# Performance work log

Measured on AMD Instinct MI355X. Metric: run time of the kernel, lower is better.

The kernel has to match this reference:

```python
import jax, jax.numpy as jnp
import numpy as np

H = 16
D_MODEL = 1024
D_K = D_MODEL // H  # 64, must equal embeddim


def setup_inputs() -> dict:
    key = jax.random.key(0)
    ks = jax.random.split(key, 20)
    B, S, D = 4, 1024, D_MODEL
    s = 0.02
    inp = {
        'query': jax.random.normal(ks[0], (B, S, D), jnp.float32),
        'key':   jax.random.normal(ks[1], (B, S, D), jnp.float32),
        'value': jax.random.normal(ks[2], (B, S, D), jnp.float32),
        'mask':  jnp.ones((B, S, S), jnp.int32),
        # four d_model x d_model projections (q, k, v, out)
        'wq': jax.random.normal(ks[3], (D, D), jnp.float32) * s, 'bq': jnp.zeros((D,), jnp.float32),
        'wk': jax.random.normal(ks[4], (D, D), jnp.float32) * s, 'bk': jnp.zeros((D,), jnp.float32),
        'wv': jax.random.normal(ks[5], (D, D), jnp.float32) * s, 'bv': jnp.zeros((D,), jnp.float32),
        'wo': jax.random.normal(ks[6], (D, D), jnp.float32) * s, 'bo': jnp.zeros((D,), jnp.float32),
        # per-head (embeddim=64) linears
        'spatial_w': jax.random.normal(ks[7], (D_K, D_K), jnp.float32) * s, 'spatial_b': jnp.zeros((D_K,), jnp.float32),
        'qproj_w':   jax.random.normal(ks[8], (D_K, D_K), jnp.float32) * s, 'qproj_b':   jnp.zeros((D_K,), jnp.float32),
        'kproj_w':   jax.random.normal(ks[9], (D_K, D_K), jnp.float32) * s, 'kproj_b':   jnp.zeros((D_K,), jnp.float32),
        'vlin_w':    jax.random.normal(ks[10], (D_K, D_K), jnp.float32) * s, 'vlin_b':    jnp.zeros((D_K,), jnp.float32),
        # channel_linear: Linear(1, 64)
        'chan_w': jax.random.normal(ks[11], (1, D_K), jnp.float32) * s, 'chan_b': jnp.zeros((D_K,), jnp.float32),
    }
    return inp


def reference(query, key, value, mask,
              wq, bq, wk, bk, wv, bv, wo, bo,
              spatial_w, spatial_b, qproj_w, qproj_b,
              kproj_w, kproj_b, vlin_w, vlin_b, chan_w, chan_b):
    B, S, D = query.shape
    # project and split heads -> [B, H, S, D_K]
    def heads(x, w, b):
        return (x @ w + b).reshape(B, S, H, D_K).transpose(0, 2, 1, 3)
    q = heads(query, wq, bq)
    k = heads(key, wk, bk)
    v = heads(value, wv, bv)

    q = jax.nn.elu(q @ spatial_w + spatial_b)
    q_refine = q @ qproj_w + qproj_b
    # channel gate: mean over channels -> Linear(1,64) -> matmul with raw key
    alpha = q_refine.mean(-1, keepdims=True) @ chan_w + chan_b        # [B,H,S,64]
    gate = jax.nn.sigmoid(jnp.einsum('bhqe,bhke->bhqk', alpha, k))    # [B,H,S,S]

    k2 = jax.nn.elu(k @ kproj_w + kproj_b)
    scores = jnp.einsum('bhqe,bhke->bhqk', q, k2) / jnp.sqrt(jnp.asarray(D_K, q.dtype))
    scores = scores * gate
    scores = jnp.where(mask[:, None] == 0, jnp.asarray(-1e9, scores.dtype), scores)
    p_attn = jax.nn.softmax(scores, axis=-1)

    v2 = jax.nn.elu(v @ vlin_w + vlin_b)
    x = jnp.einsum('bhqk,bhke->bhqe', p_attn, v2)                     # [B,H,S,64]
    x = x.transpose(0, 2, 1, 3).reshape(B, S, H * D_K)
    return x @ wo + bo
```

## Files before the change

kernel.cpp:

```cpp
#include <hip/hip_runtime.h>
#include <math.h>

#define D_MODEL 1024
#define NH 16
#define DK 64
#define S_LEN 1024
#define BATCH 4
#define MROWS (BATCH * S_LEN)

typedef short bf16x8 __attribute__((ext_vector_type(8)));
typedef float f32x4 __attribute__((ext_vector_type(4)));
typedef unsigned short u16;

__device__ __forceinline__ float elu1(float x) {
    return x > 0.f ? x : (expf(x) - 1.f);
}

__device__ __forceinline__ u16 f2bf(float f) {
    union { float f; unsigned u; } v; v.f = f;
    unsigned u = v.u;
    return (u16)((u + 0x7fffu + ((u >> 16) & 1u)) >> 16);
}

__device__ __forceinline__ unsigned pack2(float a, float b) {
    union { float f; unsigned u; } ua, ub; ua.f = a; ub.f = b;
    return ((ua.u + 0x8000u) >> 16) | ((ub.u + 0x8000u) & 0xffff0000u);
}

__device__ __forceinline__ void async16(const void* g, void* l) {
    __builtin_amdgcn_global_load_lds(
        (const __attribute__((address_space(1))) unsigned int*)g,
        (__attribute__((address_space(3))) unsigned int*)l,
        16, 0, 0);
}

__global__ __launch_bounds__(256) void cast_wt(
    const float* __restrict__ wq, const float* __restrict__ wk,
    const float* __restrict__ wv, const float* __restrict__ wo,
    u16* __restrict__ WT)
{
    __shared__ float T[64][65];
    const int z = blockIdx.z;
    const float* W = (z == 0) ? wq : ((z == 1) ? wk : ((z == 2) ? wv : wo));
    u16* O = WT + (size_t)z * D_MODEL * D_MODEL;
    const int tid = threadIdx.x;
    const int k0 = blockIdx.y * 64, n0 = blockIdx.x * 64;
    const int r = tid >> 4, c4 = (tid & 15) * 4;
    #pragma unroll
    for (int p = 0; p < 4; p++) {
        float4 v = *(const float4*)&W[(size_t)(k0 + r + p * 16) * D_MODEL + n0 + c4];
        T[r + p * 16][c4 + 0] = v.x; T[r + p * 16][c4 + 1] = v.y;
        T[r + p * 16][c4 + 2] = v.z; T[r + p * 16][c4 + 3] = v.w;
    }
    __syncthreads();
    #pragma unroll
    for (int p = 0; p < 4; p++) {
        const int i = r + p * 16;
        ushort4 o4;
        o4.x = f2bf(T[c4 + 0][i]); o4.y = f2bf(T[c4 + 1][i]);
        o4.z = f2bf(T[c4 + 2][i]); o4.w = f2bf(T[c4 + 3][i]);
        *(ushort4*)&O[(size_t)(n0 + i) * D_MODEL + k0 + c4] = o4;
    }
}

__global__ __launch_bounds__(256) void proj_fused(
    const float* __restrict__ Xq, const float* __restrict__ Xk, const float* __restrict__ Xv,
    const u16* __restrict__ WTq, const u16* __restrict__ WTk, const u16* __restrict__ WTv,
    const float* __restrict__ bq, const float* __restrict__ bk, const float* __restrict__ bv,
    const float* __restrict__ spatial_w, const float* __restrict__ spatial_b,
    const float* __restrict__ qproj_w, const float* __restrict__ qproj_b,
    const float* __restrict__ kproj_w, const float* __restrict__ kproj_b,
    const float* __restrict__ vlin_w, const float* __restrict__ vlin_b,
    const float* __restrict__ chan_w, const float* __restrict__ chan_b,
    u16* __restrict__ Qh, u16* __restrict__ K2, u16* __restrict__ V2t,
    float* __restrict__ mB, float* __restrict__ uB, float* __restrict__ vB)
{
    __shared__ __align__(16) u16 smem[23040];
    __shared__ float auxA[64];
    __shared__ float auxS;

    u16* As = smem;
    u16* Bs = smem + 8192;
    u16* W2t = smem + 18432;

    const int z = blockIdx.z;
    const float* X = (z == 0) ? Xq : ((z == 1) ? Xk : Xv);
    const u16* WT = (z == 0) ? WTq : ((z == 1) ? WTk : WTv);
    const float* B1 = (z == 0) ? bq : ((z == 1) ? bk : bv);
    const float* W2 = (z == 0) ? spatial_w : ((z == 1) ? kproj_w : vlin_w);
    const float* B2 = (z == 0) ? spatial_b : ((z == 1) ? kproj_b : vlin_b);

    const int tid = threadIdx.x;
    const int wave = tid >> 6, lane = tid & 63;
    const int col = lane & 15, quad = lane >> 4;
    const int wr = wave >> 1, wc = wave & 1;
    const int r0 = blockIdx.x * 128, n0 = blockIdx.y * 128;
    const int hh = blockIdx.y * 2 + wc;

    #pragma unroll
    for (int p = 0; p < 4; p++) {
        int idx = p * 256 + tid;
        int f = idx >> 4, e4 = (idx & 15) * 4;
        float4 w4 = *(const float4*)&W2[f * 64 + e4];
        W2t[(e4 + 0) * 72 + f] = f2bf(w4.x);
        W2t[(e4 + 1) * 72 + f] = f2bf(w4.y);
        W2t[(e4 + 2) * 72 + f] = f2bf(w4.z);
        W2t[(e4 + 3) * 72 + f] = f2bf(w4.w);
    }
    if (z == 0) {
        {
            int row = tid >> 2, part = tid & 3;
            float s = 0.f;
            for (int e = part * 16; e < part * 16 + 16; e++) s += qproj_w[row * 64 + e];
            s += __shfl_xor(s, 1);
            s += __shfl_xor(s, 2);
            if (part == 0) auxA[row] = s * (1.f / 64.f);
        }
        if (tid < 64) {
            float s = qproj_b[tid];
            #pragma unroll
            for (int m = 1; m < 64; m <<= 1) s += __shfl_xor(s, m);
            if (tid == 0) auxS = s * (1.f / 64.f);
        }
    }

    const int arow = tid >> 1, ap = tid & 1;
    const float* aptr = X + (size_t)(r0 + arow) * D_MODEL + ap * 32;
    u16* adst = As + ap * 4096 + arow * 32;

    const int brow = lane >> 2, bseg = lane & 3;
    const u16* bp = WT + (size_t)(n0 + wave * 32 + brow) * D_MODEL + bseg * 8;
    u16* bd_l0 = Bs + (wave * 32) * 32;
    u16* bd_l1 = Bs + (wave * 32 + 16) * 32;
    u16* bd_h0 = Bs + 4096 + (wave * 32) * 32;
    u16* bd_h1 = Bs + 4096 + (wave * 32 + 16) * 32;

    f32x4 acc[4][4];
    #pragma unroll
    for (int i = 0; i < 4; i++)
        #pragma unroll
        for (int j = 0; j < 4; j++)
            acc[i][j] = (f32x4){0.f, 0.f, 0.f, 0.f};

    float4 fr[8];
    #pragma unroll
    for (int i = 0; i < 8; i++) fr[i] = *(const float4*)(aptr + i * 4);

    for (int k0 = 0; k0 < D_MODEL; k0 += 64) {
        if (k0) __syncthreads();
        async16(bp + k0, bd_l0);
        async16(bp + 16 * D_MODEL + k0, bd_l1);
        async16(bp + k0 + 32, bd_h0);
        async16(bp + 16 * D_MODEL + k0 + 32, bd_h1);
        {
            #pragma unroll
            for (int j = 0; j < 4; j++) {
                uint4 q;
                q.x = pack2(fr[2 * j].x, fr[2 * j].y);
                q.y = pack2(fr[2 * j].z, fr[2 * j].w);
                q.z = pack2(fr[2 * j + 1].x, fr[2 * j + 1].y);
                q.w = pack2(fr[2 * j + 1].z, fr[2 * j + 1].w);
                *(uint4*)(adst + j * 8) = q;
            }
        }
        if (k0 + 64 < D_MODEL) {
            const float* apn = aptr + k0 + 64;
            #pragma unroll
            for (int i = 0; i < 8; i++) fr[i] = *(const float4*)(apn + i * 4);
        }
        __syncthreads();
        const u16* Abase = As + (wr * 64 + col) * 32 + quad * 8;
        const u16* Bbase = Bs + (wc * 64 + col) * 32 + quad * 8;
        #pragma unroll
        for (int p = 0; p < 2; p++) {
            bf16x8 af[4], bfr[4];
            #pragma unroll
            for (int mi = 0; mi < 4; mi++) af[mi] = *(const bf16x8*)(Abase + p * 4096 + mi * 512);
            #pragma unroll
            for (int ni = 0; ni < 4; ni++) bfr[ni] = *(const bf16x8*)(Bbase + p * 4096 + ni * 512);
            #pragma unroll
            for (int mi = 0; mi < 4; mi++)
                #pragma unroll
                for (int ni = 0; ni < 4; ni++)
                    acc[mi][ni] = __builtin_amdgcn_mfma_f32_16x16x32_bf16(af[mi], bfr[ni], acc[mi][ni], 0, 0, 0);
        }
    }

    float b1v[4];
    #pragma unroll
    for (int ni = 0; ni < 4; ni++) b1v[ni] = B1[hh * 64 + ni * 16 + col];

    const int rbase = r0 + wr * 64;
    const int b = rbase >> 10;
    const int s0 = rbase & 1023;
    const size_t svecbase = ((size_t)b * NH + hh) * S_LEN;

    if (z == 1) {
        float cw[4], cb[4];
        #pragma unroll
        for (int ni = 0; ni < 4; ni++) { cw[ni] = chan_w[ni * 16 + col]; cb[ni] = chan_b[ni * 16 + col]; }
        #pragma unroll
        for (int mi = 0; mi < 4; mi++)
            #pragma unroll
            for (int r = 0; r < 4; r++) {
                float su = 0.f, sv = 0.f;
                #pragma unroll
                for (int ni = 0; ni < 4; ni++) {
                    float p = acc[mi][ni][r] + b1v[ni];
                    su += p * cw[ni];
                    sv += p * cb[ni];
                }
                su += __shfl_xor(su, 1); su += __shfl_xor(su, 2);
                su += __shfl_xor(su, 4); su += __shfl_xor(su, 8);
                sv += __shfl_xor(sv, 1); sv += __shfl_xor(sv, 2);
                sv += __shfl_xor(sv, 4); sv += __shfl_xor(sv, 8);
                if (col == 0) {
                    const size_t idx = svecbase + s0 + mi * 16 + quad * 4 + r;
                    uB[idx] = su;
                    vB[idx] = sv;
                }
            }
    }

    __syncthreads();

    u16* Pw = smem + wave * 4608;
    #pragma unroll
    for (int mi = 0; mi < 4; mi++)
        #pragma unroll
        for (int ni = 0; ni < 4; ni++)
            #pragma unroll
            for (int r = 0; r < 4; r++)
                Pw[(mi * 16 + quad * 4 + r) * 72 + ni * 16 + col] =
                    f2bf(acc[mi][ni][r] + b1v[ni]);

    __builtin_amdgcn_s_waitcnt(0xc07f);

    bf16x8 af2[4][2], bf2r[4][2];
    #pragma unroll
    for (int mi = 0; mi < 4; mi++) {
        af2[mi][0] = *(const bf16x8*)&Pw[(mi * 16 + col) * 72 + quad * 8];
        af2[mi][1] = *(const bf16x8*)&Pw[(mi * 16 + col) * 72 + 32 + quad * 8];
    }
    #pragma unroll
    for (int ni = 0; ni < 4; ni++) {
        bf2r[ni][0] = *(const bf16x8*)&W2t[(ni * 16 + col) * 72 + quad * 8];
        bf2r[ni][1] = *(const bf16x8*)&W2t[(ni * 16 + col) * 72 + 32 + quad * 8];
    }
    f32x4 out2[4][4];
    #pragma unroll
    for (int mi = 0; mi < 4; mi++)
        #pragma unroll
        for (int ni = 0; ni < 4; ni++) {
            f32x4 c = (f32x4){0.f, 0.f, 0.f, 0.f};
            c = __builtin_amdgcn_mfma_f32_16x16x32_bf16(af2[mi][0], bf2r[ni][0], c, 0, 0, 0);
            c = __builtin_amdgcn_mfma_f32_16x16x32_bf16(af2[mi][1], bf2r[ni][1], c, 0, 0, 0);
            out2[mi][ni] = c;
        }

    float b2v[4];
    #pragma unroll
    for (int ni = 0; ni < 4; ni++) b2v[ni] = B2[ni * 16 + col];
    float qs[4][4][4];
    #pragma unroll
    for (int mi = 0; mi < 4; mi++)
        #pragma unroll
        for (int ni = 0; ni < 4; ni++)
            #pragma unroll
            for (int r = 0; r < 4; r++)
                qs[mi][ni][r] = elu1(out2[mi][ni][r] + b2v[ni]);

    if (z == 0) {
        float aw[4];
        #pragma unroll
        for (int ni = 0; ni < 4; ni++) aw[ni] = auxA[ni * 16 + col];
        #pragma unroll
        for (int mi = 0; mi < 4; mi++)
            #pragma unroll
            for (int r = 0; r < 4; r++) {
                float pm = 0.f;
                #pragma unroll
                for (int ni = 0; ni < 4; ni++) pm += qs[mi][ni][r] * aw[ni];
                pm += __shfl_xor(pm, 1); pm += __shfl_xor(pm, 2);
                pm += __shfl_xor(pm, 4); pm += __shfl_xor(pm, 8);
                if (col == 0)
                    mB[svecbase + s0 + mi * 16 + quad * 4 + r] = pm + auxS;
            }
        #pragma unroll
        for (int mi = 0; mi < 4; mi++)
            #pragma unroll
            for (int ni = 0; ni < 4; ni++)
                #pragma unroll
                for (int r = 0; r < 4; r++)
                    Qh[(size_t)(rbase + mi * 16 + quad * 4 + r) * D_MODEL
                       + hh * 64 + ni * 16 + col] = f2bf(qs[mi][ni][r] * 0.125f);
    } else if (z == 1) {
        #pragma unroll
        for (int mi = 0; mi < 4; mi++)
            #pragma unroll
            for (int ni = 0; ni < 4; ni++)
                #pragma unroll
                for (int r = 0; r < 4; r++)
                    K2[(size_t)(rbase + mi * 16 + quad * 4 + r) * D_MODEL
                       + hh * 64 + ni * 16 + col] = f2bf(qs[mi][ni][r]);
    } else {
        __builtin_amdgcn_s_waitcnt(0xc07f);
        #pragma unroll
        for (int mi = 0; mi < 4; mi++)
            #pragma unroll
            for (int ni = 0; ni < 4; ni++)
                #pragma unroll
                for (int r = 0; r < 4; r++)
                    Pw[(ni * 16 + col) * 72 + mi * 16 + quad * 4 + r] = f2bf(qs[mi][ni][r]);
        __builtin_amdgcn_s_waitcnt(0xc07f);
        const int d = lane;
        u16* dst = V2t + (((size_t)b * NH + hh) * DK + d) * S_LEN + s0;
        const u16* srcp = Pw + d * 72;
        #pragma unroll
        for (int seg = 0; seg < 8; seg++)
            *(uint4*)(dst + seg * 8) = *(const uint4*)(srcp + seg * 8);
    }
}

__global__ __launch_bounds__(256) void attn_mfma(
    const u16* __restrict__ Qh, const u16* __restrict__ K2h, const u16* __restrict__ V2t,
    const float* __restrict__ Mq, const float* __restrict__ Uk, const float* __restrict__ Vk,
    const int* __restrict__ mask, u16* __restrict__ X)
{
    __shared__ u16 K2s[2][64][72];
    __shared__ u16 V2s[2][64][72];
    __shared__ u16 Ps[4][16][72];

    const int tid = threadIdx.x;
    const int wave = tid >> 6, lane = tid & 63;
    const int col = lane & 15, quad = lane >> 4;
    const int b = blockIdx.z, h = blockIdx.y;
    const int q0 = blockIdx.x * 64;
    const size_t hb = ((size_t)(b * NH + h)) * S_LEN * DK;
    const size_t sb = ((size_t)(b * NH + h)) * S_LEN;

    bf16x8 qf0, qf1;
    {
        const u16* qp = Qh + (size_t)(b * S_LEN + q0 + wave * 16 + col) * D_MODEL + h * 64 + quad * 8;
        qf0 = *(const bf16x8*)qp;
        qf1 = *(const bf16x8*)(qp + 32);
    }
    float mqv[4];
    #pragma unroll
    for (int r = 0; r < 4; r++)
        mqv[r] = Mq[sb + q0 + wave * 16 + quad * 4 + r];

    const int srow = tid >> 2, sseg = tid & 3;
    const u16* ksrc = K2h + (size_t)(b * S_LEN + srow) * D_MODEL + h * 64 + sseg * 16;
    const u16* vsrc = V2t + hb + (size_t)srow * S_LEN + sseg * 16;
    const int* mrow = mask + (size_t)b * S_LEN * S_LEN
                    + (size_t)(q0 + wave * 16 + quad * 4) * S_LEN + col;

    uint4 ka = *(const uint4*)(ksrc);
    uint4 kb = *(const uint4*)(ksrc + 8);
    uint4 va = *(const uint4*)(vsrc);
    uint4 vb = *(const uint4*)(vsrc + 8);
    float ku[4], kv[4];
    int mk[4][4];
    #pragma unroll
    for (int nb = 0; nb < 4; nb++) {
        ku[nb] = Uk[sb + nb * 16 + col];
        kv[nb] = Vk[sb + nb * 16 + col];
        #pragma unroll
        for (int r = 0; r < 4; r++) mk[nb][r] = mrow[(size_t)r * S_LEN + nb * 16];
    }

    float psum[4] = {0.f, 0.f, 0.f, 0.f};
    f32x4 o[4];
    #pragma unroll
    for (int nb = 0; nb < 4; nb++) o[nb] = (f32x4){0.f, 0.f, 0.f, 0.f};

    for (int t = 0; t < 16; t++) {
        const int bsel = t & 1;
        *(uint4*)&K2s[bsel][srow][sseg * 16]     = ka;
        *(uint4*)&K2s[bsel][srow][sseg * 16 + 8] = kb;
        *(uint4*)&V2s[bsel][srow][sseg * 16]     = va;
        *(uint4*)&V2s[bsel][srow][sseg * 16 + 8] = vb;
        __syncthreads();

        float kun[4], kvn[4];
        int mkn[4][4];
        if (t < 15) {
            const int k1 = (t + 1) * 64;
            const u16* ks = ksrc + (size_t)k1 * D_MODEL;
            const u16* vs = vsrc + k1;
            ka = *(const uint4*)(ks);
            kb = *(const uint4*)(ks + 8);
            va = *(const uint4*)(vs);
            vb = *(const uint4*)(vs + 8);
            #pragma unroll
            for (int nb = 0; nb < 4; nb++) {
                kun[nb] = Uk[sb + k1 + nb * 16 + col];
                kvn[nb] = Vk[sb + k1 + nb * 16 + col];
                #pragma unroll
                for (int r = 0; r < 4; r++)
                    mkn[nb][r] = mrow[k1 + (size_t)r * S_LEN + nb * 16];
            }
        }

        f32x4 sc[4];
        #pragma unroll
        for (int nb = 0; nb < 4; nb++) {
            bf16x8 b0 = *(const bf16x8*)&K2s[bsel][nb * 16 + col][quad * 8];
            bf16x8 b1 = *(const bf16x8*)&K2s[bsel][nb * 16 + col][32 + quad * 8];
            f32x4 c = (f32x4){0.f, 0.f, 0.f, 0.f};
            c = __builtin_amdgcn_mfma_f32_16x16x32_bf16(qf0, b0, c, 0, 0, 0);
            c = __builtin_amdgcn_mfma_f32_16x16x32_bf16(qf1, b1, c, 0, 0, 0);
            sc[nb] = c;
        }

        #pragma unroll
        for (int nb = 0; nb < 4; nb++) {
            #pragma unroll
            for (int r = 0; r < 4; r++) {
                float g = 1.f / (1.f + __expf(-(mqv[r] * ku[nb] + kv[nb])));
                float sv = sc[nb][r] * g;
                sv = mk[nb][r] ? sv : -30.f;
                float p = __expf(sv);
                psum[r] += p;
                Ps[wave][quad * 4 + r][nb * 16 + col] = f2bf(p);
            }
        }
        __builtin_amdgcn_s_waitcnt(0xc07f);
        bf16x8 a0 = *(const bf16x8*)&Ps[wave][col][quad * 8];
        bf16x8 a1 = *(const bf16x8*)&Ps[wave][col][32 + quad * 8];

        #pragma unroll
        for (int nb = 0; nb < 4; nb++) {
            bf16x8 b0 = *(const bf16x8*)&V2s[bsel][nb * 16 + col][quad * 8];
            bf16x8 b1 = *(const bf16x8*)&V2s[bsel][nb * 16 + col][32 + quad * 8];
            o[nb] = __builtin_amdgcn_mfma_f32_16x16x32_bf16(a0, b0, o[nb], 0, 0, 0);
            o[nb] = __builtin_amdgcn_mfma_f32_16x16x32_bf16(a1, b1, o[nb], 0, 0, 0);
        }

        if (t < 15) {
            #pragma unroll
            for (int nb = 0; nb < 4; nb++) {
                ku[nb] = kun[nb]; kv[nb] = kvn[nb];
                #pragma unroll
                for (int r = 0; r < 4; r++) mk[nb][r] = mkn[nb][r];
            }
        }
    }

    #pragma unroll
    for (int r = 0; r < 4; r++) {
        float t = psum[r];
        t += __shfl_xor(t, 1);
        t += __shfl_xor(t, 2);
        t += __shfl_xor(t, 4);
        t += __shfl_xor(t, 8);
        float inv = 1.f / t;
        u16* xp = X + (size_t)(b * S_LEN + q0 + wave * 16 + quad * 4 + r) * D_MODEL + h * 64 + col;
        #pragma unroll
        for (int nb = 0; nb < 4; nb++)
            xp[nb * 16] = f2bf(o[nb][r] * inv);
    }
}

__global__ __launch_bounds__(256) void out_gemm(
    const u16* __restrict__ A, const u16* __restrict__ WT,
    const float* __restrict__ bias, float* __restrict__ C)
{
    __shared__ u16 As[128 * 32];
    __shared__ u16 Bs[128 * 32];

    const int tid = threadIdx.x;
    const int wave = tid >> 6, lane = tid & 63;
    const int col = lane & 15, quad = lane >> 4;
    const int wr = wave >> 1, wc = wave & 1;
    const int r0 = blockIdx.x * 128, n0 = blockIdx.y * 128;

    const int ch0 = 2 * wave, ch1 = 2 * wave + 1;
    const u16* aptr0 = A + (size_t)(r0 + ch0 * 16 + (lane >> 2)) * D_MODEL + (lane & 3) * 8;
    const u16* aptr1 = A + (size_t)(r0 + ch1 * 16 + (lane >> 2)) * D_MODEL + (lane & 3) * 8;
    const u16* bptr0 = WT + (size_t)(n0 + ch0 * 16 + (lane >> 2)) * D_MODEL + (lane & 3) * 8;
    const u16* bptr1 = WT + (size_t)(n0 + ch1 * 16 + (lane >> 2)) * D_MODEL + (lane & 3) * 8;
    u16* adst0 = As + ch0 * 512;
    u16* adst1 = As + ch1 * 512;
    u16* bdst0 = Bs + ch0 * 512;
    u16* bdst1 = Bs + ch1 * 512;

    f32x4 acc[4][4];
    #pragma unroll
    for (int i = 0; i < 4; i++)
        #pragma unroll
        for (int j = 0; j < 4; j++)
            acc[i][j] = (f32x4){0.f, 0.f, 0.f, 0.f};

    for (int k0 = 0; k0 < D_MODEL; k0 += 32) {
        if (k0) __syncthreads();
        async16(aptr0 + k0, adst0);
        async16(aptr1 + k0, adst1);
        async16(bptr0 + k0, bdst0);
        async16(bptr1 + k0, bdst1);
        __syncthreads();
        const u16* Ab = As + (wr * 64 + col) * 32 + quad * 8;
        const u16* Bb = Bs + (wc * 64 + col) * 32 + quad * 8;
        bf16x8 af[4], bfr[4];
        #pragma unroll
        for (int mi = 0; mi < 4; mi++) af[mi] = *(const bf16x8*)(Ab + mi * 512);
        #pragma unroll
        for (int ni = 0; ni < 4; ni++) bfr[ni] = *(const bf16x8*)(Bb + ni * 512);
        #pragma unroll
        for (int mi = 0; mi < 4; mi++)
            #pragma unroll
            for (int ni = 0; ni < 4; ni++)
                acc[mi][ni] = __builtin_amdgcn_mfma_f32_16x16x32_bf16(af[mi], bfr[ni], acc[mi][ni], 0, 0, 0);
    }

    #pragma unroll
    for (int mi = 0; mi < 4; mi++)
        #pragma unroll
        for (int ni = 0; ni < 4; ni++) {
            const int gr = r0 + wr * 64 + mi * 16 + quad * 4;
            const int gc = n0 + wc * 64 + ni * 16 + col;
            const float bb = bias[gc];
            #pragma unroll
            for (int r = 0; r < 4; r++)
                C[(size_t)(gr + r) * D_MODEL + gc] = acc[mi][ni][r] + bb;
        }
}

extern "C" void kernel_launch(void* const* d_in, const int* in_sizes, int n_in,
                              void* d_out, int out_size, void* d_ws, size_t ws_size,
                              hipStream_t stream) {
    (void)in_sizes; (void)n_in; (void)out_size; (void)ws_size;
    const float* query = (const float*)d_in[0];
    const float* key_  = (const float*)d_in[1];
    const float* value = (const float*)d_in[2];
    const int*   mask  = (const int*)d_in[3];
    const float* wq = (const float*)d_in[4];  const float* bq = (const float*)d_in[5];
    const float* wk = (const float*)d_in[6];  const float* bk = (const float*)d_in[7];
    const float* wv = (const float*)d_in[8];  const float* bv = (const float*)d_in[9];
    const float* wo = (const float*)d_in[10]; const float* bo = (const float*)d_in[11];
    const float* spatial_w = (const float*)d_in[12]; const float* spatial_b = (const float*)d_in[13];
    const float* qproj_w   = (const float*)d_in[14]; const float* qproj_b   = (const float*)d_in[15];
    const float* kproj_w   = (const float*)d_in[16]; const float* kproj_b   = (const float*)d_in[17];
    const float* vlin_w    = (const float*)d_in[18]; const float* vlin_b    = (const float*)d_in[19];
    const float* chan_w    = (const float*)d_in[20]; const float* chan_b    = (const float*)d_in[21];
    float* out = (float*)d_out;

    char* ws = (char*)d_ws;
    u16* Qh  = (u16*)ws;
    u16* K2  = (u16*)(ws + ((size_t)8  << 20));
    u16* Xb  = (u16*)(ws + ((size_t)16 << 20));
    u16* WT  = (u16*)(ws + ((size_t)24 << 20));
    u16* V2t = (u16*)(ws + ((size_t)32 << 20));
    float* mB = (float*)(ws + ((size_t)40 << 20));
    float* uB = mB + (size_t)BATCH * NH * S_LEN;
    float* vB = uB + (size_t)BATCH * NH * S_LEN;
    const size_t WSZ = (size_t)D_MODEL * D_MODEL;

    cast_wt<<<dim3(16, 16, 4), 256, 0, stream>>>(wq, wk, wv, wo, WT);
    proj_fused<<<dim3(32, 8, 3), 256, 0, stream>>>(query, key_, value,
        WT, WT + WSZ, WT + 2 * WSZ, bq, bk, bv,
        spatial_w, spatial_b, qproj_w, qproj_b, kproj_w, kproj_b,
        vlin_w, vlin_b, chan_w, chan_b,
        Qh, K2, V2t, mB, uB, vB);
    attn_mfma<<<dim3(S_LEN / 64, NH, BATCH), 256, 0, stream>>>(Qh, K2, V2t, mB, uB, vB, mask, Xb);
    out_gemm<<<dim3(32, 8), 256, 0, stream>>>(Xb, WT + 3 * WSZ, bo, out);
}
```

Baseline: 317.3 us.

## Replace async LDS loads with register-prefetched tiles and widen out_gemm K-step

Drops the global_load_lds async copies in the projection GEMM and the output GEMM. Each thread now loads the next K-tile of weights and activations into registers after the barrier, so the global loads overlap the MFMA work on the current tile, then writes them to LDS at the top of the next iteration. out_gemm also moves from 32-wide to 64-wide K-steps, which halves its barrier count and doubles its LDS tiles. The cost is more register pressure and an explicit LDS store pass in place of direct-to-LDS loads.

```diff
diff --git a/kernel.cpp b/kernel.cpp
--- a/kernel.cpp
+++ b/kernel.cpp
@@ -25,13 +25,6 @@
 __device__ __forceinline__ unsigned pack2(float a, float b) {
     union { float f; unsigned u; } ua, ub; ua.f = a; ub.f = b;
     return ((ua.u + 0x8000u) >> 16) | ((ub.u + 0x8000u) & 0xffff0000u);
-}
-
-__device__ __forceinline__ void async16(const void* g, void* l) {
-    __builtin_amdgcn_global_load_lds(
-        (const __attribute__((address_space(1))) unsigned int*)g,
-        (__attribute__((address_space(3))) unsigned int*)l,
-        16, 0, 0);
 }
 
 __global__ __launch_bounds__(256) void cast_wt(
@@ -128,12 +121,8 @@
     const float* aptr = X + (size_t)(r0 + arow) * D_MODEL + ap * 32;
     u16* adst = As + ap * 4096 + arow * 32;
 
-    const int brow = lane >> 2, bseg = lane & 3;
-    const u16* bp = WT + (size_t)(n0 + wave * 32 + brow) * D_MODEL + bseg * 8;
-    u16* bd_l0 = Bs + (wave * 32) * 32;
-    u16* bd_l1 = Bs + (wave * 32 + 16) * 32;
-    u16* bd_h0 = Bs + 4096 + (wave * 32) * 32;
-    u16* bd_h1 = Bs + 4096 + (wave * 32 + 16) * 32;
+    const u16* bsrc = WT + (size_t)(n0 + arow) * D_MODEL + ap * 32;
+    u16* bdst = Bs + ap * 4096 + arow * 32;
 
     f32x4 acc[4][4];
     #pragma unroll
@@ -143,32 +132,36 @@
             acc[i][j] = (f32x4){0.f, 0.f, 0.f, 0.f};
 
     float4 fr[8];
+    uint4 bu[4];
     #pragma unroll
     for (int i = 0; i < 8; i++) fr[i] = *(const float4*)(aptr + i * 4);
+    #pragma unroll
+    for (int i = 0; i < 4; i++) bu[i] = *(const uint4*)(bsrc + i * 8);
 
     for (int k0 = 0; k0 < D_MODEL; k0 += 64) {
         if (k0) __syncthreads();
-        async16(bp + k0, bd_l0);
-        async16(bp + 16 * D_MODEL + k0, bd_l1);
-        async16(bp + k0 + 32, bd_h0);
-        async16(bp + 16 * D_MODEL + k0 + 32, bd_h1);
-        {
-            #pragma unroll
-            for (int j = 0; j < 4; j++) {
-                uint4 q;
-                q.x = pack2(fr[2 * j].x, fr[2 * j].y);
-                q.y = pack2(fr[2 * j].z, fr[2 * j].w);
-                q.z = pack2(fr[2 * j + 1].x, fr[2 * j + 1].y);
-                q.w = pack2(fr[2 * j + 1].z, fr[2 * j + 1].w);
-                *(uint4*)(adst + j * 8) = q;
-            }
-        }
+        #pragma unroll
+        for (int j = 0; j < 4; j++) {
+            uint4 q;
+            q.x = pack2(fr[2 * j].x, fr[2 * j].y);
+            q.y = pack2(fr[2 * j].z, fr[2 * j].w);
+            q.z = pack2(fr[2 * j + 1].x, fr[2 * j + 1].y);
+            q.w = pack2(fr[2 * j + 1].z, fr[2 * j + 1].w);
+            *(uint4*)(adst + j * 8) = q;
+        }
+        #pragma unroll
+        for (int i = 0; i < 4; i++) *(uint4*)(bdst + i * 8) = bu[i];
+        __syncthreads();
+
         if (k0 + 64 < D_MODEL) {
             const float* apn = aptr + k0 + 64;
             #pragma unroll
             for (int i = 0; i < 8; i++) fr[i] = *(const float4*)(apn + i * 4);
-        }
-        __syncthreads();
+            const u16* bpn = bsrc + k0 + 64;
+            #pragma unroll
+            for (int i = 0; i < 4; i++) bu[i] = *(const uint4*)(bpn + i * 8);
+        }
+
         const u16* Abase = As + (wr * 64 + col) * 32 + quad * 8;
         const u16* Bbase = Bs + (wc * 64 + col) * 32 + quad * 8;
         #pragma unroll
@@ -467,8 +460,8 @@
     const u16* __restrict__ A, const u16* __restrict__ WT,
     const float* __restrict__ bias, float* __restrict__ C)
 {
-    __shared__ u16 As[128 * 32];
-    __shared__ u16 Bs[128 * 32];
+    __shared__ u16 As[8192];
+    __shared__ u16 Bs[8192];
 
     const int tid = threadIdx.x;
     const int wave = tid >> 6, lane = tid & 63;
@@ -476,15 +469,11 @@
     const int wr = wave >> 1, wc = wave & 1;
     const int r0 = blockIdx.x * 128, n0 = blockIdx.y * 128;
 
-    const int ch0 = 2 * wave, ch1 = 2 * wave + 1;
-    const u16* aptr0 = A + (size_t)(r0 + ch0 * 16 + (lane >> 2)) * D_MODEL + (lane & 3) * 8;
-    const u16* aptr1 = A + (size_t)(r0 + ch1 * 16 + (lane >> 2)) * D_MODEL + (lane & 3) * 8;
-    const u16* bptr0 = WT + (size_t)(n0 + ch0 * 16 + (lane >> 2)) * D_MODEL + (lane & 3) * 8;
-    const u16* bptr1 = WT + (size_t)(n0 + ch1 * 16 + (lane >> 2)) * D_MODEL + (lane & 3) * 8;
-    u16* adst0 = As + ch0 * 512;
-    u16* adst1 = As + ch1 * 512;
-    u16* bdst0 = Bs + ch0 * 512;
-    u16* bdst1 = Bs + ch1 * 512;
+    const int arow = tid >> 1, ap = tid & 1;
+    const u16* asrc = A + (size_t)(r0 + arow) * D_MODEL + ap * 32;
+    const u16* bsrc = WT + (size_t)(n0 + arow) * D_MODEL + ap * 32;
+    u16* adst = As + ap * 4096 + arow * 32;
+    u16* bdst = Bs + ap * 4096 + arow * 32;
 
     f32x4 acc[4][4];
     #pragma unroll
@@ -493,25 +482,44 @@
         for (int j = 0; j < 4; j++)
             acc[i][j] = (f32x4){0.f, 0.f, 0.f, 0.f};
 
-    for (int k0 = 0; k0 < D_MODEL; k0 += 32) {
+    uint4 au[4], bu[4];
+    #pragma unroll
+    for (int i = 0; i < 4; i++) au[i] = *(const uint4*)(asrc + i * 8);
+    #pragma unroll
+    for (int i = 0; i < 4; i++) bu[i] = *(const uint4*)(bsrc + i * 8);
+
+    for (int k0 = 0; k0 < D_MODEL; k0 += 64) {
         if (k0) __syncthreads();
-        async16(aptr0 + k0, adst0);
-        async16(aptr1 + k0, adst1);
-        async16(bptr0 + k0, bdst0);
-        async16(bptr1 + k0, bdst1);
+        #pragma unroll
+        for (int i = 0; i < 4; i++) *(uint4*)(adst + i * 8) = au[i];
+        #pragma unroll
+        for (int i = 0; i < 4; i++) *(uint4*)(bdst + i * 8) = bu[i];
         __syncthreads();
-        const u16* Ab = As + (wr * 64 + col) * 32 + quad * 8;
-        const u16* Bb = Bs + (wc * 64 + col) * 32 + quad * 8;
-        bf16x8 af[4], bfr[4];
-        #pragma unroll
-        for (int mi = 0; mi < 4; mi++) af[mi] = *(const bf16x8*)(Ab + mi * 512);
-        #pragma unroll
-        for (int ni = 0; ni < 4; ni++) bfr[ni] = *(const bf16x8*)(Bb + ni * 512);
-        #pragma unroll
-        for (int mi = 0; mi < 4; mi++)
-            #pragma unroll
-            for (int ni = 0; ni < 4; ni++)
-                acc[mi][ni] = __builtin_amdgcn_mfma_f32_16x16x32_bf16(af[mi], bfr[ni], acc[mi][ni], 0, 0, 0);
+
+        if (k0 + 64 < D_MODEL) {
+            const u16* apn = asrc + k0 + 64;
+            const u16* bpn = bsrc + k0 + 64;
+            #pragma unroll
+            for (int i = 0; i < 4; i++) au[i] = *(const uint4*)(apn + i * 8);
+            #pragma unroll
+            for (int i = 0; i < 4; i++) bu[i] = *(const uint4*)(bpn + i * 8);
+        }
+
+        const u16* Abase = As + (wr * 64 + col) * 32 + quad * 8;
+        const u16* Bbase = Bs + (wc * 64 + col) * 32 + quad * 8;
+        #pragma unroll
+        for (int p = 0; p < 2; p++) {
+            bf16x8 af[4], bfr[4];
+            #pragma unroll
+            for (int mi = 0; mi < 4; mi++) af[mi] = *(const bf16x8*)(Abase + p * 4096 + mi * 512);
+            #pragma unroll
+            for (int ni = 0; ni < 4; ni++) bfr[ni] = *(const bf16x8*)(Bbase + p * 4096 + ni * 512);
+            #pragma unroll
+            for (int mi = 0; mi < 4; mi++)
+                #pragma unroll
+                for (int ni = 0; ni < 4; ni++)
+                    acc[mi][ni] = __builtin_amdgcn_mfma_f32_16x16x32_bf16(af[mi], bfr[ni], acc[mi][ni], 0, 0, 0);
+        }
     }
 
     #pragma unroll
```

After: 375.4 us. +18.3%, slower.

## Shrink projection and output GEMM tiles to raise block count and occupancy

Applied to the files above, without the earlier changes.

The fused projection kernel now computes a 128x64 tile per block (one head) instead of 128x128, with K-step 32 and smaller LDS. The per-head 64x64 linear and the V transpose are reworked to process 16-row chunks per wave and stage through shared memory in two passes. The output GEMM goes from 128x128 tiles to 64x64 tiles, launching four times as many blocks. This is meant to improve occupancy and wave count on the many-CU GPU, at the cost of less data reuse per block and more barriers per K step.

```diff
diff --git a/kernel.cpp b/kernel.cpp
--- a/kernel.cpp
+++ b/kernel.cpp
@@ -75,13 +75,13 @@
     u16* __restrict__ Qh, u16* __restrict__ K2, u16* __restrict__ V2t,
     float* __restrict__ mB, float* __restrict__ uB, float* __restrict__ vB)
 {
-    __shared__ __align__(16) u16 smem[23040];
+    __shared__ __align__(16) u16 smem[10752];
     __shared__ float auxA[64];
     __shared__ float auxS;
 
     u16* As = smem;
-    u16* Bs = smem + 8192;
-    u16* W2t = smem + 18432;
+    u16* Bs = smem + 4096;
+    u16* W2t = smem + 6144;
 
     const int z = blockIdx.z;
     const float* X = (z == 0) ? Xq : ((z == 1) ? Xk : Xv);
@@ -93,9 +93,9 @@
     const int tid = threadIdx.x;
     const int wave = tid >> 6, lane = tid & 63;
     const int col = lane & 15, quad = lane >> 4;
-    const int wr = wave >> 1, wc = wave & 1;
-    const int r0 = blockIdx.x * 128, n0 = blockIdx.y * 128;
-    const int hh = blockIdx.y * 2 + wc;
+    const int r0 = blockIdx.x * 128;
+    const int hh = blockIdx.y;
+    const int n0 = hh * 64;
 
     #pragma unroll
     for (int p = 0; p < 4; p++) {
@@ -124,75 +124,63 @@
         }
     }
 
-    const int arow = tid >> 1, ap = tid & 1;
-    const float* aptr = X + (size_t)(r0 + arow) * D_MODEL + ap * 32;
-    u16* adst = As + ap * 4096 + arow * 32;
-
-    const int brow = lane >> 2, bseg = lane & 3;
-    const u16* bp = WT + (size_t)(n0 + wave * 32 + brow) * D_MODEL + bseg * 8;
-    u16* bd_l0 = Bs + (wave * 32) * 32;
-    u16* bd_l1 = Bs + (wave * 32 + 16) * 32;
-    u16* bd_h0 = Bs + 4096 + (wave * 32) * 32;
-    u16* bd_h1 = Bs + 4096 + (wave * 32 + 16) * 32;
-
-    f32x4 acc[4][4];
-    #pragma unroll
-    for (int i = 0; i < 4; i++)
+    const int arow = tid >> 1, ahalf = tid & 1;
+    const float* aptr = X + (size_t)(r0 + arow) * D_MODEL + ahalf * 16;
+    u16* adst = As + arow * 32 + ahalf * 16;
+
+    const u16* bp = WT + (size_t)(n0 + wave * 16 + (lane >> 2)) * D_MODEL + (lane & 3) * 8;
+    u16* bdst = Bs + wave * 16 * 32;
+
+    f32x4 acc[2][4];
+    #pragma unroll
+    for (int i = 0; i < 2; i++)
         #pragma unroll
         for (int j = 0; j < 4; j++)
             acc[i][j] = (f32x4){0.f, 0.f, 0.f, 0.f};
 
-    float4 fr[8];
-    #pragma unroll
-    for (int i = 0; i < 8; i++) fr[i] = *(const float4*)(aptr + i * 4);
-
-    for (int k0 = 0; k0 < D_MODEL; k0 += 64) {
+    float4 fr[4];
+    #pragma unroll
+    for (int i = 0; i < 4; i++) fr[i] = *(const float4*)(aptr + i * 4);
+
+    for (int k0 = 0; k0 < D_MODEL; k0 += 32) {
         if (k0) __syncthreads();
-        async16(bp + k0, bd_l0);
-        async16(bp + 16 * D_MODEL + k0, bd_l1);
-        async16(bp + k0 + 32, bd_h0);
-        async16(bp + 16 * D_MODEL + k0 + 32, bd_h1);
+        async16(bp + k0, bdst);
         {
-            #pragma unroll
-            for (int j = 0; j < 4; j++) {
-                uint4 q;
-                q.x = pack2(fr[2 * j].x, fr[2 * j].y);
-                q.y = pack2(fr[2 * j].z, fr[2 * j].w);
-                q.z = pack2(fr[2 * j + 1].x, fr[2 * j + 1].y);
-                q.w = pack2(fr[2 * j + 1].z, fr[2 * j + 1].w);
-                *(uint4*)(adst + j * 8) = q;
-            }
-        }
-        if (k0 + 64 < D_MODEL) {
-            const float* apn = aptr + k0 + 64;
-            #pragma unroll
-            for (int i = 0; i < 8; i++) fr[i] = *(const float4*)(apn + i * 4);
+            uint4 q0, q1;
+            q0.x = pack2(fr[0].x, fr[0].y); q0.y = pack2(fr[0].z, fr[0].w);
+            q0.z = pack2(fr[1].x, fr[1].y); q0.w = pack2(fr[1].z, fr[1].w);
+            q1.x = pack2(fr[2].x, fr[2].y); q1.y = pack2(fr[2].z, fr[2].w);
+            q1.z = pack2(fr[3].x, fr[3].y); q1.w = pack2(fr[3].z, fr[3].w);
+            *(uint4*)adst = q0;
+            *(uint4*)(adst + 8) = q1;
+        }
+        if (k0 + 32 < D_MODEL) {
+            const float* ap = aptr + k0 + 32;
+            #pragma unroll
+            for (int i = 0; i < 4; i++) fr[i] = *(const float4*)(ap + i * 4);
         }
         __syncthreads();
-        const u16* Abase = As + (wr * 64 + col) * 32 + quad * 8;
-        const u16* Bbase = Bs + (wc * 64 + col) * 32 + quad * 8;
-        #pragma unroll
-        for (int p = 0; p < 2; p++) {
-            bf16x8 af[4], bfr[4];
-            #pragma unroll
-            for (int mi = 0; mi < 4; mi++) af[mi] = *(const bf16x8*)(Abase + p * 4096 + mi * 512);
-            #pragma unroll
-            for (int ni = 0; ni < 4; ni++) bfr[ni] = *(const bf16x8*)(Bbase + p * 4096 + ni * 512);
-            #pragma unroll
-            for (int mi = 0; mi < 4; mi++)
-                #pragma unroll
-                for (int ni = 0; ni < 4; ni++)
-                    acc[mi][ni] = __builtin_amdgcn_mfma_f32_16x16x32_bf16(af[mi], bfr[ni], acc[mi][ni], 0, 0, 0);
-        }
+        const u16* Abase = As + (wave * 32 + col) * 32 + quad * 8;
+        const u16* Bbase = Bs + col * 32 + quad * 8;
+        bf16x8 af[2], bfr[4];
+        #pragma unroll
+        for (int mi = 0; mi < 2; mi++) af[mi] = *(const bf16x8*)(Abase + mi * 512);
+        #pragma unroll
+        for (int ni = 0; ni < 4; ni++) bfr[ni] = *(const bf16x8*)(Bbase + ni * 512);
+        #pragma unroll
+        for (int mi = 0; mi < 2; mi++)
+            #pragma unroll
+            for (int ni = 0; ni < 4; ni++)
+                acc[mi][ni] = __builtin_amdgcn_mfma_f32_16x16x32_bf16(af[mi], bfr[ni], acc[mi][ni], 0, 0, 0);
     }
 
     float b1v[4];
     #pragma unroll
-    for (int ni = 0; ni < 4; ni++) b1v[ni] = B1[hh * 64 + ni * 16 + col];
-
-    const int rbase = r0 + wr * 64;
-    const int b = rbase >> 10;
-    const int s0 = rbase & 1023;
+    for (int ni = 0; ni < 4; ni++) b1v[ni] = B1[n0 + ni * 16 + col];
+
+    const int rbase = r0 + wave * 32;
+    const int b = r0 >> 10;
+    const int s0 = (r0 & 1023) + wave * 32;
     const size_t svecbase = ((size_t)b * NH + hh) * S_LEN;
 
     if (z == 1) {
@@ -200,7 +188,7 @@
         #pragma unroll
         for (int ni = 0; ni < 4; ni++) { cw[ni] = chan_w[ni * 16 + col]; cb[ni] = chan_b[ni * 16 + col]; }
         #pragma unroll
-        for (int mi = 0; mi < 4; mi++)
+        for (int mi = 0; mi < 2; mi++)
             #pragma unroll
             for (int r = 0; r < 4; r++) {
                 float su = 0.f, sv = 0.f;
@@ -224,58 +212,42 @@
 
     __syncthreads();
 
-    u16* Pw = smem + wave * 4608;
-    #pragma unroll
-    for (int mi = 0; mi < 4; mi++)
-        #pragma unroll
-        for (int ni = 0; ni < 4; ni++)
-            #pragma unroll
-            for (int r = 0; r < 4; r++)
-                Pw[(mi * 16 + quad * 4 + r) * 72 + ni * 16 + col] =
-                    f2bf(acc[mi][ni][r] + b1v[ni]);
-
-    __builtin_amdgcn_s_waitcnt(0xc07f);
-
-    bf16x8 af2[4][2], bf2r[4][2];
-    #pragma unroll
-    for (int mi = 0; mi < 4; mi++) {
-        af2[mi][0] = *(const bf16x8*)&Pw[(mi * 16 + col) * 72 + quad * 8];
-        af2[mi][1] = *(const bf16x8*)&Pw[(mi * 16 + col) * 72 + 32 + quad * 8];
-    }
+    u16* Pchunk = smem + wave * 1536;
+    bf16x8 bf2r[4][2];
     #pragma unroll
     for (int ni = 0; ni < 4; ni++) {
         bf2r[ni][0] = *(const bf16x8*)&W2t[(ni * 16 + col) * 72 + quad * 8];
         bf2r[ni][1] = *(const bf16x8*)&W2t[(ni * 16 + col) * 72 + 32 + quad * 8];
     }
-    f32x4 out2[4][4];
-    #pragma unroll
-    for (int mi = 0; mi < 4; mi++)
+    float qs[2][4][4];
+    #pragma unroll
+    for (int mi = 0; mi < 2; mi++) {
+        #pragma unroll
+        for (int ni = 0; ni < 4; ni++)
+            #pragma unroll
+            for (int r = 0; r < 4; r++)
+                Pchunk[(quad * 4 + r) * 72 + ni * 16 + col] = f2bf(acc[mi][ni][r] + b1v[ni]);
+        __builtin_amdgcn_s_waitcnt(0xc07f);
+        bf16x8 a0 = *(const bf16x8*)&Pchunk[col * 72 + quad * 8];
+        bf16x8 a1 = *(const bf16x8*)&Pchunk[col * 72 + 32 + quad * 8];
+        __builtin_amdgcn_s_waitcnt(0xc07f);
         #pragma unroll
         for (int ni = 0; ni < 4; ni++) {
             f32x4 c = (f32x4){0.f, 0.f, 0.f, 0.f};
-            c = __builtin_amdgcn_mfma_f32_16x16x32_bf16(af2[mi][0], bf2r[ni][0], c, 0, 0, 0);
-            c = __builtin_amdgcn_mfma_f32_16x16x32_bf16(af2[mi][1], bf2r[ni][1], c, 0, 0, 0);
-            out2[mi][ni] = c;
-        }
-
-    float b2v[4];
-    #pragma unroll
-    for (int ni = 0; ni < 4; ni++) b2v[ni] = B2[ni * 16 + col];
-    float qs[4][4][4];
-    #pragma unroll
-    for (int mi = 0; mi < 4; mi++)
-        #pragma unroll
-        for (int ni = 0; ni < 4; ni++)
-            #pragma unroll
-            for (int r = 0; r < 4; r++)
-                qs[mi][ni][r] = elu1(out2[mi][ni][r] + b2v[ni]);
+            c = __builtin_amdgcn_mfma_f32_16x16x32_bf16(a0, bf2r[ni][0], c, 0, 0, 0);
+            c = __builtin_amdgcn_mfma_f32_16x16x32_bf16(a1, bf2r[ni][1], c, 0, 0, 0);
+            const float bb = B2[ni * 16 + col];
+            #pragma unroll
+            for (int r = 0; r < 4; r++) qs[mi][ni][r] = elu1(c[r] + bb);
+        }
+    }
 
     if (z == 0) {
         float aw[4];
         #pragma unroll
         for (int ni = 0; ni < 4; ni++) aw[ni] = auxA[ni * 16 + col];
         #pragma unroll
-        for (int mi = 0; mi < 4; mi++)
+        for (int mi = 0; mi < 2; mi++)
             #pragma unroll
             for (int r = 0; r < 4; r++) {
                 float pm = 0.f;
@@ -287,38 +259,48 @@
                     mB[svecbase + s0 + mi * 16 + quad * 4 + r] = pm + auxS;
             }
         #pragma unroll
-        for (int mi = 0; mi < 4; mi++)
+        for (int mi = 0; mi < 2; mi++)
             #pragma unroll
             for (int ni = 0; ni < 4; ni++)
                 #pragma unroll
                 for (int r = 0; r < 4; r++)
                     Qh[(size_t)(rbase + mi * 16 + quad * 4 + r) * D_MODEL
-                       + hh * 64 + ni * 16 + col] = f2bf(qs[mi][ni][r] * 0.125f);
+                       + n0 + ni * 16 + col] = f2bf(qs[mi][ni][r] * 0.125f);
     } else if (z == 1) {
         #pragma unroll
-        for (int mi = 0; mi < 4; mi++)
+        for (int mi = 0; mi < 2; mi++)
             #pragma unroll
             for (int ni = 0; ni < 4; ni++)
                 #pragma unroll
                 for (int r = 0; r < 4; r++)
                     K2[(size_t)(rbase + mi * 16 + quad * 4 + r) * D_MODEL
-                       + hh * 64 + ni * 16 + col] = f2bf(qs[mi][ni][r]);
+                       + n0 + ni * 16 + col] = f2bf(qs[mi][ni][r]);
     } else {
-        __builtin_amdgcn_s_waitcnt(0xc07f);
-        #pragma unroll
-        for (int mi = 0; mi < 4; mi++)
-            #pragma unroll
-            for (int ni = 0; ni < 4; ni++)
-                #pragma unroll
-                for (int r = 0; r < 4; r++)
-                    Pw[(ni * 16 + col) * 72 + mi * 16 + quad * 4 + r] = f2bf(qs[mi][ni][r]);
-        __builtin_amdgcn_s_waitcnt(0xc07f);
-        const int d = lane;
-        u16* dst = V2t + (((size_t)b * NH + hh) * DK + d) * S_LEN + s0;
-        const u16* srcp = Pw + d * 72;
-        #pragma unroll
-        for (int seg = 0; seg < 8; seg++)
-            *(uint4*)(dst + seg * 8) = *(const uint4*)(srcp + seg * 8);
+        u16* Tb = W2t;
+        __syncthreads();
+        #pragma unroll
+        for (int p = 0; p < 2; p++) {
+            if ((wave >> 1) == p) {
+                const int sloc = (wave & 1) * 32;
+                #pragma unroll
+                for (int mi = 0; mi < 2; mi++)
+                    #pragma unroll
+                    for (int ni = 0; ni < 4; ni++)
+                        #pragma unroll
+                        for (int r = 0; r < 4; r++)
+                            Tb[(ni * 16 + col) * 72 + sloc + mi * 16 + quad * 4 + r] =
+                                f2bf(qs[mi][ni][r]);
+            }
+            __syncthreads();
+            {
+                const int d = tid >> 2, seg = tid & 3;
+                u16* dst = V2t + (((size_t)b * NH + hh) * DK + d) * S_LEN
+                         + (r0 & 1023) + p * 64 + seg * 16;
+                *(uint4*)dst = *(const uint4*)&Tb[d * 72 + seg * 16];
+                *(uint4*)(dst + 8) = *(const uint4*)&Tb[d * 72 + seg * 16 + 8];
+            }
+            if (p == 0) __syncthreads();
+        }
     }
 }
 
@@ -467,64 +449,48 @@
     const u16* __restrict__ A, const u16* __restrict__ WT,
     const float* __restrict__ bias, float* __restrict__ C)
 {
-    __shared__ u16 As[128 * 32];
-    __shared__ u16 Bs[128 * 32];
+    __shared__ u16 As[64 * 32];
+    __shared__ u16 Bs[64 * 32];
 
     const int tid = threadIdx.x;
     const int wave = tid >> 6, lane = tid & 63;
     const int col = lane & 15, quad = lane >> 4;
-    const int wr = wave >> 1, wc = wave & 1;
-    const int r0 = blockIdx.x * 128, n0 = blockIdx.y * 128;
-
-    const int ch0 = 2 * wave, ch1 = 2 * wave + 1;
-    const u16* aptr0 = A + (size_t)(r0 + ch0 * 16 + (lane >> 2)) * D_MODEL + (lane & 3) * 8;
-    const u16* aptr1 = A + (size_t)(r0 + ch1 * 16 + (lane >> 2)) * D_MODEL + (lane & 3) * 8;
-    const u16* bptr0 = WT + (size_t)(n0 + ch0 * 16 + (lane >> 2)) * D_MODEL + (lane & 3) * 8;
-    const u16* bptr1 = WT + (size_t)(n0 + ch1 * 16 + (lane >> 2)) * D_MODEL + (lane & 3) * 8;
-    u16* adst0 = As + ch0 * 512;
-    u16* adst1 = As + ch1 * 512;
-    u16* bdst0 = Bs + ch0 * 512;
-    u16* bdst1 = Bs + ch1 * 512;
-
-    f32x4 acc[4][4];
-    #pragma unroll
-    for (int i = 0; i < 4; i++)
-        #pragma unroll
-        for (int j = 0; j < 4; j++)
-            acc[i][j] = (f32x4){0.f, 0.f, 0.f, 0.f};
+    const int r0 = blockIdx.x * 64, n0 = blockIdx.y * 64;
+
+    const u16* ap = A + (size_t)(r0 + wave * 16 + (lane >> 2)) * D_MODEL + (lane & 3) * 8;
+    const u16* bp = WT + (size_t)(n0 + wave * 16 + (lane >> 2)) * D_MODEL + (lane & 3) * 8;
+    u16* adst = As + wave * 16 * 32;
+    u16* bdst = Bs + wave * 16 * 32;
+
+    f32x4 acc[4];
+    #pragma unroll
+    for (int j = 0; j < 4; j++) acc[j] = (f32x4){0.f, 0.f, 0.f, 0.f};
 
     for (int k0 = 0; k0 < D_MODEL; k0 += 32) {
         if (k0) __syncthreads();
-        async16(aptr0 + k0, adst0);
-        async16(aptr1 + k0, adst1);
-        async16(bptr0 + k0, bdst0);
-        async16(bptr1 + k0, bdst1);
+        async16(ap + k0, adst);
+        async16(bp + k0, bdst);
         __syncthreads();
-        const u16* Ab = As + (wr * 64 + col) * 32 + quad * 8;
-        const u16* Bb = Bs + (wc * 64 + col) * 32 + quad * 8;
-        bf16x8 af[4], bfr[4];
-        #pragma unroll
-        for (int mi = 0; mi < 4; mi++) af[mi] = *(const bf16x8*)(Ab + mi * 512);
+        const u16* Ab = As + (wave * 16 + col) * 32 + quad * 8;
+        const u16* Bb = Bs + col * 32 + quad * 8;
+        bf16x8 af = *(const bf16x8*)Ab;
+        bf16x8 bfr[4];
         #pragma unroll
         for (int ni = 0; ni < 4; ni++) bfr[ni] = *(const bf16x8*)(Bb + ni * 512);
         #pragma unroll
-        for (int mi = 0; mi < 4; mi++)
-            #pragma unroll
-            for (int ni = 0; ni < 4; ni++)
-                acc[mi][ni] = __builtin_amdgcn_mfma_f32_16x16x32_bf16(af[mi], bfr[ni], acc[mi][ni], 0, 0, 0);
-    }
-
-    #pragma unroll
-    for (int mi = 0; mi < 4; mi++)
-        #pragma unroll
-        for (int ni = 0; ni < 4; ni++) {
-            const int gr = r0 + wr * 64 + mi * 16 + quad * 4;
-            const int gc = n0 + wc * 64 + ni * 16 + col;
-            const float bb = bias[gc];
-            #pragma unroll
-            for (int r = 0; r < 4; r++)
-                C[(size_t)(gr + r) * D_MODEL + gc] = acc[mi][ni][r] + bb;
-        }
+        for (int ni = 0; ni < 4; ni++)
+            acc[ni] = __builtin_amdgcn_mfma_f32_16x16x32_bf16(af, bfr[ni], acc[ni], 0, 0, 0);
+    }
+
+    #pragma unroll
+    for (int ni = 0; ni < 4; ni++) {
+        const int gr = r0 + wave * 16 + quad * 4;
+        const int gc = n0 + ni * 16 + col;
+        const float bb = bias[gc];
+        #pragma unroll
+        for (int r = 0; r < 4; r++)
+            C[(size_t)(gr + r) * D_MODEL + gc] = acc[ni][r] + bb;
+    }
 }
 
 extern "C" void kernel_launch(void* const* d_in, const int* in_sizes, int n_in,
@@ -558,11 +524,11 @@
     const size_t WSZ = (size_t)D_MODEL * D_MODEL;
 
     cast_wt<<<dim3(16, 16, 4), 256, 0, stream>>>(wq, wk, wv, wo, WT);
-    proj_fused<<<dim3(32, 8, 3), 256, 0, stream>>>(query, key_, value,
+    proj_fused<<<dim3(32, 16, 3), 256, 0, stream>>>(query, key_, value,
         WT, WT + WSZ, WT + 2 * WSZ, bq, bk, bv,
         spatial_w, spatial_b, qproj_w, qproj_b, kproj_w, kproj_b,
         vlin_w, vlin_b, chan_w, chan_b,
         Qh, K2, V2t, mB, uB, vB);
     attn_mfma<<<dim3(S_LEN / 64, NH, BATCH), 256, 0, stream>>>(Qh, K2, V2t, mB, uB, vB, mask, Xb);
-    out_gemm<<<dim3(32, 8), 256, 0, stream>>>(Xb, WT + 3 * WSZ, bo, out);
-}
+    out_gemm<<<dim3(64, 16), 256, 0, stream>>>(Xb, WT + 3 * WSZ, bo, out);
+}
```

After: 314.3 us. No clear change (-1.0%).
